# Performance work log

Measured on AMD Instinct MI355X. Metric: run time of the kernel, lower is better.

Reference implementation:

```python
import jax, jax.numpy as jnp
import numpy as np

D_MODEL = 1024
NUM_HEADS = 16
HEAD_DIM = D_MODEL // NUM_HEADS
THETA = 10000.0


def _rope(x):
    # x: [B, H, S, Dk]; interleaved even/odd rotation as in the torch module
    *_, seq_len, d_k = x.shape
    d = d_k // 2
    inv_freq = 1.0 / (THETA ** (2.0 * jnp.arange(d, dtype=jnp.float32) / d_k))
    pos = jnp.arange(seq_len, dtype=jnp.float32)
    angles = pos[:, None] * inv_freq[None, :]  # [S, d]
    cos = jnp.cos(angles)
    sin = jnp.sin(angles)
    x_even = x[..., 0::2]
    x_odd = x[..., 1::2]
    rot_even = x_even * cos - x_odd * sin
    rot_odd = x_even * sin + x_odd * cos
    return jnp.stack([rot_even, rot_odd], axis=-1).reshape(x.shape)


def setup_inputs() -> dict:
    key = jax.random.key(0)
    ks = jax.random.split(key, 5)
    B, S = 4, 2048
    x = jax.random.normal(ks[0], (B, S, D_MODEL), dtype=jnp.float32)
    q_w = jax.random.uniform(ks[1], (D_MODEL, D_MODEL), dtype=jnp.float32)
    k_w = jax.random.uniform(ks[2], (D_MODEL, D_MODEL), dtype=jnp.float32)
    v_w = jax.random.uniform(ks[3], (D_MODEL, D_MODEL), dtype=jnp.float32)
    o_w = jax.random.uniform(ks[4], (D_MODEL, D_MODEL), dtype=jnp.float32)
    return {"x": x, "q_w": q_w, "k_w": k_w, "v_w": v_w, "o_w": o_w}


def reference(x, q_w, k_w, v_w, o_w):
    B, S, _ = x.shape
    def split_heads(t):
        return t.reshape(B, S, NUM_HEADS, HEAD_DIM).transpose(0, 2, 1, 3)  # [B,H,S,Dk]
    Q = split_heads(x @ q_w.T)
    K = split_heads(x @ k_w.T)
    V = split_heads(x @ v_w.T)
    Q = _rope(Q)
    K = _rope(K)
    scale = 1.0 / jnp.sqrt(jnp.float32(HEAD_DIM))
    scores = jnp.einsum('bhqd,bhkd->bhqk', Q, K) * scale  # [B,H,S,S]
    causal = jnp.tril(jnp.ones((S, S), dtype=bool))
    scores = jnp.where(causal[None, None], scores, -jnp.inf)
    attn = jax.nn.softmax(scores, axis=-1)
    out = jnp.einsum('bhqk,bhkd->bhqd', attn, V)  # [B,H,S,Dk]
    out = out.transpose(0, 2, 1, 3).reshape(B, S, D_MODEL)
    return out @ o_w.T
```

## Files before the change

### kernel.cpp

```cpp
#include <hip/hip_runtime.h>
#include <hip/hip_bf16.h>
#include <cstdint>
#include <cstddef>

#define D_MODEL   1024
#define NUM_HEADS 16
#define HEAD_DIM  64
#define SEQ       2048
#define BATCH     4
#define BH        (BATCH*NUM_HEADS)
#define MROWS     (BATCH*SEQ)

typedef _Float16 half8  __attribute__((ext_vector_type(8)));
typedef _Float16 half4v __attribute__((ext_vector_type(4)));
typedef float    floatx4 __attribute__((ext_vector_type(4)));

__device__ inline void gld_lds16(const void* g, void* l) {
    __builtin_amdgcn_global_load_lds(
        (__attribute__((address_space(1))) void*)g,
        (__attribute__((address_space(3))) void*)l,
        16, 0, 0);
}

__global__ void rope_table(float2* __restrict__ tab) {
    const int i = blockIdx.x * blockDim.x + threadIdx.x;
    const int p = i & 31, s = i >> 5;
    const double inv = pow(10000.0, -(double)p / 32.0);
    const double ang = (double)s * inv;
    tab[i] = make_float2((float)cos(ang), (float)sin(ang));
}

__global__ void f32_split_f16(const float* __restrict__ in,
                              _Float16* __restrict__ hi,
                              _Float16* __restrict__ lo, int n4) {
    int i = blockIdx.x * blockDim.x + threadIdx.x;
    if (i >= n4) return;
    float4 v = ((const float4*)in)[i];
    half4v h = { (_Float16)v.x, (_Float16)v.y, (_Float16)v.z, (_Float16)v.w };
    half4v l = { (_Float16)(v.x - (float)h.x), (_Float16)(v.y - (float)h.y),
                 (_Float16)(v.z - (float)h.z), (_Float16)(v.w - (float)h.w) };
    ((half4v*)hi)[i] = h;
    ((half4v*)lo)[i] = l;
}

__global__ void conv_weights(const float* __restrict__ qw, const float* __restrict__ kw,
                             const float* __restrict__ vw, const float* __restrict__ ow,
                             _Float16* __restrict__ qwh, _Float16* __restrict__ qwl,
                             _Float16* __restrict__ kwh, _Float16* __restrict__ kwl,
                             _Float16* __restrict__ vwh, _Float16* __restrict__ owh) {
    const int i = blockIdx.x * blockDim.x + threadIdx.x;
    const int which = i >> 18;
    const int j = i & 262143;
    const float4 v = ((const float4*)(which == 0 ? qw : which == 1 ? kw :
                                      which == 2 ? vw : ow))[j];
    half4v h = { (_Float16)v.x, (_Float16)v.y, (_Float16)v.z, (_Float16)v.w };
    if (which < 2) {
        half4v l = { (_Float16)(v.x - (float)h.x), (_Float16)(v.y - (float)h.y),
                     (_Float16)(v.z - (float)h.z), (_Float16)(v.w - (float)h.w) };
        ((half4v*)(which ? kwh : qwh))[j] = h;
        ((half4v*)(which ? kwl : qwl))[j] = l;
    } else {
        ((half4v*)(which == 2 ? vwh : owh))[j] = h;
    }
}

__global__ __launch_bounds__(256)
void gemm_bt(const _Float16* __restrict__ A, const _Float16* __restrict__ B,
             float* __restrict__ Cout, int M, int N, int K) {
    __shared__ _Float16 As[128*32];
    __shared__ _Float16 Bs[128*32];

    const int nb = N >> 7;
    const int bx = blockIdx.x % nb;
    const int by = blockIdx.x / nb;
    const int m0 = by << 7, n0 = bx << 7;

    const int t    = threadIdx.x;
    const int w    = t >> 6;
    const int lane = t & 63;
    const int r    = lane & 15;
    const int quad = lane >> 4;
    const int wm   = (w >> 1) << 6;
    const int wn   = (w & 1) << 6;

    const int srow = lane >> 2;
    const int scol = (lane & 3) << 3;

    floatx4 acc[4][4];
    #pragma unroll
    for (int i = 0; i < 4; i++)
        #pragma unroll
        for (int j = 0; j < 4; j++)
            acc[i][j] = (floatx4){0.f, 0.f, 0.f, 0.f};

    for (int k0 = 0; k0 < K; k0 += 32) {
        __syncthreads();
        #pragma unroll
        for (int p = 0; p < 2; ++p) {
            const int rbase = p*64 + w*16;
            gld_lds16(&A[(size_t)(m0 + rbase + srow)*K + k0 + scol], &As[rbase*32]);
            gld_lds16(&B[(size_t)(n0 + rbase + srow)*K + k0 + scol], &Bs[rbase*32]);
        }
        __syncthreads();

        half8 af[4], bf[4];
        #pragma unroll
        for (int i = 0; i < 4; i++)
            af[i] = *(const half8*)&As[(wm + i*16 + r)*32 + quad*8];
        #pragma unroll
        for (int j = 0; j < 4; j++)
            bf[j] = *(const half8*)&Bs[(wn + j*16 + r)*32 + quad*8];

        #pragma unroll
        for (int i = 0; i < 4; i++)
            #pragma unroll
            for (int j = 0; j < 4; j++)
                acc[i][j] = __builtin_amdgcn_mfma_f32_16x16x32_f16(
                                af[i], bf[j], acc[i][j], 0, 0, 0);
    }

    #pragma unroll
    for (int i = 0; i < 4; i++)
        #pragma unroll
        for (int j = 0; j < 4; j++)
            #pragma unroll
            for (int v = 0; v < 4; v++) {
                const int m = m0 + wm + i*16 + quad*4 + v;
                const int n = n0 + wn + j*16 + r;
                Cout[(size_t)m*N + n] = acc[i][j][v];
            }
}

__global__ __launch_bounds__(256)
void gemm_qkv(const _Float16* __restrict__ Axh, const _Float16* __restrict__ Axl,
              const _Float16* __restrict__ qwh, const _Float16* __restrict__ qwl,
              const _Float16* __restrict__ kwh, const _Float16* __restrict__ kwl,
              const _Float16* __restrict__ vwh,
              _Float16* __restrict__ Qhi, _Float16* __restrict__ Qlo,
              _Float16* __restrict__ Khi, _Float16* __restrict__ Klo,
              _Float16* __restrict__ Vt,  const float2* __restrict__ tab) {
    __shared__ _Float16 smem[4*4096];
    _Float16* Ash = smem;
    _Float16* Asl = smem + 4096;
    _Float16* Bsh = smem + 8192;
    _Float16* Bsl = smem + 12288;

    const int bxa = blockIdx.x;
    const int bx  = bxa % 24;
    const int by  = bxa / 24;
    const int wt  = bx >> 3;
    const int n0  = (bx & 7) << 7;
    const int m0  = by << 7;

    const _Float16* Bh = (wt == 0) ? qwh : (wt == 1) ? kwh : vwh;
    const _Float16* Bl = (wt == 0) ? qwl : kwl;

    const int t    = threadIdx.x;
    const int w    = t >> 6;
    const int lane = t & 63;
    const int r    = lane & 15;
    const int quad = lane >> 4;
    const int wm   = (w >> 1) << 6;
    const int wn   = (w & 1) << 6;

    const int srow = lane >> 2;
    const int scol = (lane & 3) << 3;

    floatx4 acc[4][4];
    #pragma unroll
    for (int i = 0; i < 4; i++)
        #pragma unroll
        for (int j = 0; j < 4; j++)
            acc[i][j] = (floatx4){0.f, 0.f, 0.f, 0.f};

    for (int k0 = 0; k0 < 1024; k0 += 32) {
        __syncthreads();
        #pragma unroll
        for (int p = 0; p < 2; ++p) {
            const int rbase = p*64 + w*16;
            const size_t ga = (size_t)(m0 + rbase + srow)*1024 + k0 + scol;
            const size_t gb = (size_t)(n0 + rbase + srow)*1024 + k0 + scol;
            gld_lds16(&Axh[ga], &Ash[rbase*32]);
            gld_lds16(&Bh [gb], &Bsh[rbase*32]);
            if (wt < 2) {
                gld_lds16(&Axl[ga], &Asl[rbase*32]);
                gld_lds16(&Bl [gb], &Bsl[rbase*32]);
            }
        }
        __syncthreads();

        half8 ah[4], bh[4];
        #pragma unroll
        for (int i = 0; i < 4; i++)
            ah[i] = *(const half8*)&Ash[(wm + i*16 + r)*32 + quad*8];
        #pragma unroll
        for (int j = 0; j < 4; j++)
            bh[j] = *(const half8*)&Bsh[(wn + j*16 + r)*32 + quad*8];

        if (wt < 2) {
            half8 al[4], bl[4];
            #pragma unroll
            for (int i = 0; i < 4; i++)
                al[i] = *(const half8*)&Asl[(wm + i*16 + r)*32 + quad*8];
            #pragma unroll
            for (int j = 0; j < 4; j++)
                bl[j] = *(const half8*)&Bsl[(wn + j*16 + r)*32 + quad*8];
            #pragma unroll
            for (int i = 0; i < 4; i++)
                #pragma unroll
                for (int j = 0; j < 4; j++) {
                    acc[i][j] = __builtin_amdgcn_mfma_f32_16x16x32_f16(
                                    ah[i], bh[j], acc[i][j], 0, 0, 0);
                    acc[i][j] = __builtin_amdgcn_mfma_f32_16x16x32_f16(
                                    ah[i], bl[j], acc[i][j], 0, 0, 0);
                    acc[i][j] = __builtin_amdgcn_mfma_f32_16x16x32_f16(
                                    al[i], bh[j], acc[i][j], 0, 0, 0);
                }
        } else {
            #pragma unroll
            for (int i = 0; i < 4; i++)
                #pragma unroll
                for (int j = 0; j < 4; j++)
                    acc[i][j] = __builtin_amdgcn_mfma_f32_16x16x32_f16(
                                    ah[i], bh[j], acc[i][j], 0, 0, 0);
        }
    }

    __syncthreads();
    float* sc = (float*)smem + w*1088;
    const int g  = lane & 7;
    const int rw = lane >> 3;
    const int hh = (n0 + wn) >> 6;

    if (wt < 2) {
        _Float16* Chi = wt ? Khi : Qhi;
        _Float16* Clo = wt ? Klo : Qlo;
        #pragma unroll
        for (int i = 0; i < 4; i++) {
            #pragma unroll
            for (int j = 0; j < 4; j++)
                #pragma unroll
                for (int v = 0; v < 4; v++)
                    sc[(quad*4 + v)*68 + j*16 + r] = acc[i][j][v];
            #pragma unroll
            for (int rg = 0; rg < 2; rg++) {
                const int row = rw + rg*8;
                const int m   = m0 + wm + i*16 + row;
                const int bb  = m >> 11, s_ = m & 2047;
                const float4 va = *(const float4*)&sc[row*68 + g*8];
                const float4 vb = *(const float4*)&sc[row*68 + g*8 + 4];
                const float vv[8] = {va.x, va.y, va.z, va.w,
                                     vb.x, vb.y, vb.z, vb.w};
                half8 hv, lv;
                #pragma unroll
                for (int p2 = 0; p2 < 4; p2++) {
                    const float2 cs = tab[s_*32 + g*4 + p2];
                    const float e0 = vv[2*p2], o0 = vv[2*p2+1];
                    const float re = e0*cs.x - o0*cs.y;
                    const float ro = e0*cs.y + o0*cs.x;
                    const _Float16 rh = (_Float16)re;
                    const _Float16 oh = (_Float16)ro;
                    hv[2*p2]   = rh; lv[2*p2]   = (_Float16)(re - (float)rh);
                    hv[2*p2+1] = oh; lv[2*p2+1] = (_Float16)(ro - (float)oh);
                }
                const size_t idx = ((((size_t)bb*NUM_HEADS + hh)*SEQ + s_) << 6) + g*8;
                *(half8*)&Chi[idx] = hv;
                *(half8*)&Clo[idx] = lv;
            }
        }
    } else {
        const int d = lane;
        #pragma unroll
        for (int i = 0; i < 4; i++) {
            #pragma unroll
            for (int j = 0; j < 4; j++)
                #pragma unroll
                for (int v = 0; v < 4; v++)
                    sc[(quad*4 + v)*68 + j*16 + r] = acc[i][j][v];
            #pragma unroll
            for (int rg = 0; rg < 2; rg++) {
                const int m  = m0 + wm + i*16 + rg*8;
                const int bb = m >> 11, s_ = m & 2047;
                half8 ov;
                #pragma unroll
                for (int rr = 0; rr < 8; rr++)
                    ov[rr] = (_Float16)sc[(rg*8 + rr)*68 + d];
                *(half8*)&Vt[((((size_t)bb*NUM_HEADS + hh)*HEAD_DIM + d) << 11) + s_] = ov;
            }
        }
    }
}

#define PSTR 72
__global__ __launch_bounds__(256)
void flash_attn(const _Float16* __restrict__ Qhi, const _Float16* __restrict__ Qlo,
                const _Float16* __restrict__ Khi, const _Float16* __restrict__ Klo,
                const _Float16* __restrict__ Vt,  _Float16* __restrict__ AO) {
    __shared__ _Float16 SB[2][6][64*32];
    __shared__ _Float16 Pl[4][16*PSTR];

    const int t    = threadIdx.x;
    const int w    = t >> 6;
    const int lane = t & 63;
    const int r    = lane & 15;
    const int quad = lane >> 4;

    const int bx = blockIdx.x;
    const int bh = bx & 63;
    const int qb = 15 - (bx >> 6);
    const int Q0 = qb << 7;
    const int q0a = Q0 + w*16;
    const int q0b = Q0 + 64 + w*16;
    const int b  = bh >> 4, h = bh & 15;

    const _Float16* Qh_ = Qhi + (size_t)bh * SEQ * HEAD_DIM;
    const _Float16* Ql_ = Qlo + (size_t)bh * SEQ * HEAD_DIM;
    const _Float16* Khg = Khi + (size_t)bh * SEQ * HEAD_DIM;
    const _Float16* Klg = Klo + (size_t)bh * SEQ * HEAD_DIM;
    const _Float16* Vtg = Vt  + (size_t)bh * HEAD_DIM * SEQ;

    half8 qh0[2], ql0[2], qh1[2], ql1[2];
    #pragma unroll
    for (int c = 0; c < 2; ++c) {
        qh0[c] = *(const half8*)&Qh_[(size_t)(q0a + r)*64 + c*32 + quad*8];
        ql0[c] = *(const half8*)&Ql_[(size_t)(q0a + r)*64 + c*32 + quad*8];
        qh1[c] = *(const half8*)&Qh_[(size_t)(q0b + r)*64 + c*32 + quad*8];
        ql1[c] = *(const half8*)&Ql_[(size_t)(q0b + r)*64 + c*32 + quad*8];
    }

    floatx4 ot0[4], ot1[4];
    #pragma unroll
    for (int dt = 0; dt < 4; ++dt) {
        ot0[dt] = (floatx4){0.f,0.f,0.f,0.f};
        ot1[dt] = (floatx4){0.f,0.f,0.f,0.f};
    }
    float mi0 = -1e30f, li0 = 0.f, mi1 = -1e30f, li1 = 0.f;

    const int sr = lane >> 2;
    const int sc = (lane & 3) << 3;
    const int rb = w << 4;

    auto stage = [&](int buf, int kt) {
        const int k0  = kt << 6;
        const int row = rb + sr;
        const size_t kr = (size_t)(k0 + row)*64;
        gld_lds16(&Khg[kr +      sc], &SB[buf][0][rb*32]);
        gld_lds16(&Khg[kr + 32 + sc], &SB[buf][1][rb*32]);
        gld_lds16(&Klg[kr +      sc], &SB[buf][2][rb*32]);
        gld_lds16(&Klg[kr + 32 + sc], &SB[buf][3][rb*32]);
        const size_t vr = (size_t)row*SEQ + k0;
        gld_lds16(&Vtg[vr +      sc], &SB[buf][4][rb*32]);
        gld_lds16(&Vtg[vr + 32 + sc], &SB[buf][5][rb*32]);
    };

    const int niter = 2*qb + 2;
    stage(0, 0);
    int cur = 0;

    for (int kt = 0; kt < niter; ++kt) {
        const int k0 = kt << 6;

        __syncthreads();
        if (kt + 1 < niter) stage(cur ^ 1, kt + 1);

        const _Float16* Kh0 = SB[cur][0];
        const _Float16* Kh1 = SB[cur][1];
        const _Float16* Kl0 = SB[cur][2];
        const _Float16* Kl1 = SB[cur][3];
        const _Float16* Vp0 = SB[cur][4];
        const _Float16* Vp1 = SB[cur][5];

        auto group = [&](int q0g, const half8 (&qhg)[2], const half8 (&qlg)[2],
                         floatx4 (&og)[4], float &mig, float &lig, bool domask) {
            float s[16];
            __builtin_amdgcn_s_setprio(1);
            #pragma unroll
            for (int sub = 0; sub < 4; ++sub) {
                floatx4 a = (floatx4){0.f,0.f,0.f,0.f};
                const int fr = (sub*16 + r)*32 + quad*8;
                const half8 kh0 = *(const half8*)&Kh0[fr];
                const half8 kh1 = *(const half8*)&Kh1[fr];
                const half8 kl0 = *(const half8*)&Kl0[fr];
                const half8 kl1 = *(const half8*)&Kl1[fr];
                a = __builtin_amdgcn_mfma_f32_16x16x32_f16(kh0, qhg[0], a, 0, 0, 0);
                a = __builtin_amdgcn_mfma_f32_16x16x32_f16(kh1, qhg[1], a, 0, 0, 0);
                a = __builtin_amdgcn_mfma_f32_16x16x32_f16(kh0, qlg[0], a, 0, 0, 0);
                a = __builtin_amdgcn_mfma_f32_16x16x32_f16(kh1, qlg[1], a, 0, 0, 0);
                a = __builtin_amdgcn_mfma_f32_16x16x32_f16(kl0, qhg[0], a, 0, 0, 0);
                a = __builtin_amdgcn_mfma_f32_16x16x32_f16(kl1, qhg[1], a, 0, 0, 0);
                #pragma unroll
                for (int v = 0; v < 4; ++v) s[sub*4 + v] = a[v] * 0.125f;
            }
            __builtin_amdgcn_s_setprio(0);

            if (domask) {
                #pragma unroll
                for (int sub = 0; sub < 4; ++sub)
                    #pragma unroll
                    for (int v = 0; v < 4; ++v)
                        if (k0 + sub*16 + quad*4 + v > q0g + r)
                            s[sub*4 + v] = -1e30f;
            }

            float tm = s[0];
            #pragma unroll
            for (int i = 1; i < 16; ++i) tm = fmaxf(tm, s[i]);
            tm = fmaxf(tm, __shfl_xor(tm, 16));
            tm = fmaxf(tm, __shfl_xor(tm, 32));
            const float mn = fmaxf(mig, tm);
            const float alpha = __expf(mig - mn);
            mig = mn;
            float rs = 0.f;
            #pragma unroll
            for (int i = 0; i < 16; ++i) { s[i] = __expf(s[i] - mn); rs += s[i]; }
            rs += __shfl_xor(rs, 16);
            rs += __shfl_xor(rs, 32);
            lig = lig*alpha + rs;
            #pragma unroll
            for (int dt = 0; dt < 4; ++dt)
                #pragma unroll
                for (int v = 0; v < 4; ++v) og[dt][v] *= alpha;

            #pragma unroll
            for (int sub = 0; sub < 4; ++sub) {
                half4v pk = { (_Float16)s[sub*4+0], (_Float16)s[sub*4+1],
                              (_Float16)s[sub*4+2], (_Float16)s[sub*4+3] };
                *(half4v*)&Pl[w][r*PSTR + sub*16 + quad*4] = pk;
            }

            __builtin_amdgcn_s_setprio(1);
            #pragma unroll
            for (int c = 0; c < 2; ++c) {
                const half8 pf = *(const half8*)&Pl[w][r*PSTR + c*32 + quad*8];
                const _Float16* Vsc = c ? Vp1 : Vp0;
                #pragma unroll
                for (int dt = 0; dt < 4; ++dt) {
                    const half8 vf = *(const half8*)&Vsc[(dt*16 + r)*32 + quad*8];
                    og[dt] = __builtin_amdgcn_mfma_f32_16x16x32_f16(vf, pf, og[dt], 0, 0, 0);
                }
            }
            __builtin_amdgcn_s_setprio(0);
        };

        if (kt <= 2*qb) group(q0a, qh0, ql0, ot0, mi0, li0, kt == 2*qb);
        group(q0b, qh1, ql1, ot1, mi1, li1, kt == 2*qb + 1);

        cur ^= 1;
    }

    {
        const float inv0 = 1.0f / li0;
        const int q = q0a + r;
        #pragma unroll
        for (int dt = 0; dt < 4; ++dt) {
            half4v o = { (_Float16)(ot0[dt][0]*inv0), (_Float16)(ot0[dt][1]*inv0),
                         (_Float16)(ot0[dt][2]*inv0), (_Float16)(ot0[dt][3]*inv0) };
            *(half4v*)&AO[((size_t)(b*SEQ + q))*D_MODEL + h*HEAD_DIM + dt*16 + quad*4] = o;
        }
    }
    {
        const float inv1 = 1.0f / li1;
        const int q = q0b + r;
        #pragma unroll
        for (int dt = 0; dt < 4; ++dt) {
            half4v o = { (_Float16)(ot1[dt][0]*inv1), (_Float16)(ot1[dt][1]*inv1),
                         (_Float16)(ot1[dt][2]*inv1), (_Float16)(ot1[dt][3]*inv1) };
            *(half4v*)&AO[((size_t)(b*SEQ + q))*D_MODEL + h*HEAD_DIM + dt*16 + quad*4] = o;
        }
    }
}

extern "C" void kernel_launch(void* const* d_in, const int* in_sizes, int n_in,
                              void* d_out, int out_size, void* d_ws, size_t ws_size,
                              hipStream_t stream) {
    const float* x  = (const float*)d_in[0];
    const float* qw = (const float*)d_in[1];
    const float* kw = (const float*)d_in[2];
    const float* vw = (const float*)d_in[3];
    const float* ow = (const float*)d_in[4];
    float* out = (float*)d_out;

    _Float16* xh  = (_Float16*)d_ws;
    _Float16* xl  = xh  + (size_t)MROWS * D_MODEL;
    _Float16* qwh = xl  + (size_t)MROWS * D_MODEL;
    _Float16* qwl = qwh + (size_t)D_MODEL * D_MODEL;
    _Float16* kwh = qwl + (size_t)D_MODEL * D_MODEL;
    _Float16* kwl = kwh + (size_t)D_MODEL * D_MODEL;
    _Float16* vwh = kwl + (size_t)D_MODEL * D_MODEL;
    _Float16* owh = vwh + (size_t)D_MODEL * D_MODEL;
    _Float16* Qhi = owh + (size_t)D_MODEL * D_MODEL;
    _Float16* Qlo = Qhi + (size_t)MROWS * D_MODEL;
    _Float16* Khi = Qlo + (size_t)MROWS * D_MODEL;
    _Float16* Klo = Khi + (size_t)MROWS * D_MODEL;
    _Float16* Vt  = Klo + (size_t)MROWS * D_MODEL;
    _Float16* AO  = Vt  + (size_t)MROWS * D_MODEL;
    float2*   tab = (float2*)(AO + (size_t)MROWS * D_MODEL);

    rope_table<<<(SEQ*32)/256, 256, 0, stream>>>(tab);

    const int nx4 = MROWS * D_MODEL / 4;
    f32_split_f16<<<nx4/256, 256, 0, stream>>>(x, xh, xl, nx4);
    conv_weights<<<(4*262144)/256, 256, 0, stream>>>(qw, kw, vw, ow,
                                                     qwh, qwl, kwh, kwl, vwh, owh);

    gemm_qkv<<<64*24, 256, 0, stream>>>(xh, xl, qwh, qwl, kwh, kwl, vwh,
                                        Qhi, Qlo, Khi, Klo, Vt, tab);

    flash_attn<<<BH * (SEQ/128), 256, 0, stream>>>(Qhi, Qlo, Khi, Klo, Vt, AO);

    gemm_bt<<<(MROWS/128)*(D_MODEL/128), 256, 0, stream>>>(AO, owh, out,
                                                           MROWS, D_MODEL, D_MODEL);
}
```

Baseline: 384.8 us.

## Overlap next K-tile global-to-LDS loads with MFMA and remap blocks for XCDs

Both GEMM kernels now load fragments from LDS into registers, synchronize, then issue the next K-tile's global-to-LDS loads before running the MFMAs. This lets the memory traffic for the next tile overlap with compute while still using a single LDS buffer. Block indices are also remapped so consecutive tiles land on the same XCD, which is meant to improve L2 reuse. The cost is a longer live range for the fragment registers, which may reduce occupancy, and correctness relies on the barrier placement.

```diff
diff --git a/kernel.cpp b/kernel.cpp
--- a/kernel.cpp
+++ b/kernel.cpp
@@ -70,9 +70,13 @@
     __shared__ _Float16 As[128*32];
     __shared__ _Float16 Bs[128*32];
 
-    const int nb = N >> 7;
-    const int bx = blockIdx.x % nb;
-    const int by = blockIdx.x / nb;
+    const int nb  = N >> 7;
+    const int nwg = gridDim.x;
+    int lb = blockIdx.x;
+    if ((nwg & 7) == 0)
+        lb = (blockIdx.x & 7) * (nwg >> 3) + (blockIdx.x >> 3);
+    const int bx = lb % nb;
+    const int by = lb / nb;
     const int m0 = by << 7, n0 = bx << 7;
 
     const int t    = threadIdx.x;
@@ -93,15 +97,18 @@
         for (int j = 0; j < 4; j++)
             acc[i][j] = (floatx4){0.f, 0.f, 0.f, 0.f};
 
+    auto stageAB = [&](int kk) {
+        #pragma unroll
+        for (int p = 0; p < 2; ++p) {
+            const int rbase = p*64 + w*16;
+            gld_lds16(&A[(size_t)(m0 + rbase + srow)*K + kk + scol], &As[rbase*32]);
+            gld_lds16(&B[(size_t)(n0 + rbase + srow)*K + kk + scol], &Bs[rbase*32]);
+        }
+    };
+
+    stageAB(0);
     for (int k0 = 0; k0 < K; k0 += 32) {
         __syncthreads();
-        #pragma unroll
-        for (int p = 0; p < 2; ++p) {
-            const int rbase = p*64 + w*16;
-            gld_lds16(&A[(size_t)(m0 + rbase + srow)*K + k0 + scol], &As[rbase*32]);
-            gld_lds16(&B[(size_t)(n0 + rbase + srow)*K + k0 + scol], &Bs[rbase*32]);
-        }
-        __syncthreads();
 
         half8 af[4], bf[4];
         #pragma unroll
@@ -110,6 +117,9 @@
         #pragma unroll
         for (int j = 0; j < 4; j++)
             bf[j] = *(const half8*)&Bs[(wn + j*16 + r)*32 + quad*8];
+
+        __syncthreads();
+        if (k0 + 32 < K) stageAB(k0 + 32);
 
         #pragma unroll
         for (int i = 0; i < 4; i++)
@@ -145,9 +155,9 @@
     _Float16* Bsh = smem + 8192;
     _Float16* Bsl = smem + 12288;
 
-    const int bxa = blockIdx.x;
-    const int bx  = bxa % 24;
-    const int by  = bxa / 24;
+    const int lb  = (blockIdx.x & 7) * 192 + (blockIdx.x >> 3);
+    const int bx  = lb % 24;
+    const int by  = lb / 24;
     const int wt  = bx >> 3;
     const int n0  = (bx & 7) << 7;
     const int m0  = by << 7;
@@ -173,13 +183,12 @@
         for (int j = 0; j < 4; j++)
             acc[i][j] = (floatx4){0.f, 0.f, 0.f, 0.f};
 
-    for (int k0 = 0; k0 < 1024; k0 += 32) {
-        __syncthreads();
+    auto stage_k = [&](int kk) {
         #pragma unroll
         for (int p = 0; p < 2; ++p) {
             const int rbase = p*64 + w*16;
-            const size_t ga = (size_t)(m0 + rbase + srow)*1024 + k0 + scol;
-            const size_t gb = (size_t)(n0 + rbase + srow)*1024 + k0 + scol;
+            const size_t ga = (size_t)(m0 + rbase + srow)*1024 + kk + scol;
+            const size_t gb = (size_t)(n0 + rbase + srow)*1024 + kk + scol;
             gld_lds16(&Axh[ga], &Ash[rbase*32]);
             gld_lds16(&Bh [gb], &Bsh[rbase*32]);
             if (wt < 2) {
@@ -187,24 +196,32 @@
                 gld_lds16(&Bl [gb], &Bsl[rbase*32]);
             }
         }
+    };
+
+    stage_k(0);
+    for (int k0 = 0; k0 < 1024; k0 += 32) {
         __syncthreads();
 
-        half8 ah[4], bh[4];
+        half8 ah[4], bh[4], al[4], bl[4];
         #pragma unroll
         for (int i = 0; i < 4; i++)
             ah[i] = *(const half8*)&Ash[(wm + i*16 + r)*32 + quad*8];
         #pragma unroll
         for (int j = 0; j < 4; j++)
             bh[j] = *(const half8*)&Bsh[(wn + j*16 + r)*32 + quad*8];
-
         if (wt < 2) {
-            half8 al[4], bl[4];
             #pragma unroll
             for (int i = 0; i < 4; i++)
                 al[i] = *(const half8*)&Asl[(wm + i*16 + r)*32 + quad*8];
             #pragma unroll
             for (int j = 0; j < 4; j++)
                 bl[j] = *(const half8*)&Bsl[(wn + j*16 + r)*32 + quad*8];
+        }
+
+        __syncthreads();
+        if (k0 + 32 < 1024) stage_k(k0 + 32);
+
+        if (wt < 2) {
             #pragma unroll
             for (int i = 0; i < 4; i++)
                 #pragma unroll
```

New measurement: 368.8 us. 4.2% less time.
